# Optimization experiments

Measured on AMD Instinct MI355X. Metric: run time of the kernel, lower is better.

Reference implementation:

```python
import jax, jax.numpy as jnp
import numpy as np

STAGE = 100  # number of weight bins


def _bin_reconstruct(w, affine):
    # Faithful vectorization of the 100-iter binning loop: element in bin i
    # (half-open interval) gets scaled by affine[i]; the max element falls
    # outside every bin (w < wmin + stage*range/stage fails) and is zeroed.
    flat = w.reshape(-1)
    wmin, wmax = flat.min(), flat.max()
    idx = jnp.floor((flat - wmin) / (wmax - wmin) * STAGE).astype(jnp.int32)
    mask = (idx < STAGE).astype(flat.dtype)  # mask is detached in torch (non-diff anyway)
    scale = affine[jnp.clip(idx, 0, STAGE - 1)]
    return flat * scale * mask


def _kl_vs_laplace(new_flat, lap):
    # F.kl_div(log_softmax(w), softmax(lap), reduction='none').mean()
    logq = jax.nn.log_softmax(new_flat)
    p = jax.nn.softmax(lap)
    return (p * (jnp.log(p) - logq)).mean()


def _adder2d(x, w, stride, padding, groups=1):
    # AdderNet conv: out = -sum_k |patch_k - w_k| (no bias)
    O, Cg, kh, kw = w.shape
    patches = jax.lax.conv_general_dilated_patches(
        x, (kh, kw), (stride, stride), [(padding, padding), (padding, padding)])
    B, _, Hp, Wp = patches.shape  # channel dim ordered (C, kh, kw), C-major
    if groups == 1:
        p = patches.reshape(B, 1, Cg * kh * kw, Hp, Wp)
        wf = w.reshape(1, O, Cg * kh * kw, 1, 1)
    else:  # depthwise: groups == C_in, Cg == 1, O == C_in
        p = patches.reshape(B, O, kh * kw, Hp, Wp)
        wf = w.reshape(1, O, kh * kw, 1, 1)
    return -jnp.abs(p - wf).sum(axis=2)  # [B, O, Hp, Wp]


def _bn_train(x, g, b, eps=1e-5):
    # BatchNorm2d in training mode (batch statistics, biased variance)
    m = x.mean(axis=(0, 2, 3), keepdims=True)
    v = ((x - m) ** 2).mean(axis=(0, 2, 3), keepdims=True)
    return (x - m) * jax.lax.rsqrt(v + eps) * g.reshape(1, -1, 1, 1) + b.reshape(1, -1, 1, 1)


def _forward(x, sw_ds, sw_c1, sw_c2, sw_c3, a_ds, a_c1, a_c2, a_c3, peg_w,
             g1, b1, g2, b2, g3, b3, gds, bds, lap_ds, lap_c1, lap_c2, lap_c3):
    kl = jnp.float32(0.0)
    f_ds = _bin_reconstruct(sw_ds, a_ds)
    kl = kl + _kl_vs_laplace(f_ds, lap_ds)
    f_c1 = _bin_reconstruct(sw_c1, a_c1)
    kl = kl + _kl_vs_laplace(f_c1, lap_c1)
    residual = jax.nn.relu(_bn_train(_adder2d(x, f_ds.reshape(sw_ds.shape), 1, 0), gds, bds))
    h = _adder2d(x, f_c1.reshape(sw_c1.shape), 1, 0)
    h = _adder2d(h, peg_w, 1, 1, groups=peg_w.shape[0])  # PEG depthwise 3x3
    h = jax.nn.relu(_bn_train(h, g1, b1))
    f_c2 = _bin_reconstruct(sw_c2, a_c2)
    kl = kl + _kl_vs_laplace(f_c2, lap_c2)
    h = _adder2d(h, f_c2.reshape(sw_c2.shape), 1, 1)
    h = jax.nn.relu(_bn_train(h, g2, b2))
    f_c3 = _bin_reconstruct(sw_c3, a_c3)
    kl = kl + _kl_vs_laplace(f_c3, lap_c3)
    h = _adder2d(h, f_c3.reshape(sw_c3.shape), 1, 0)
    h = _bn_train(h, g3, b3)  # bn3 gamma zero-initialized
    return jax.nn.relu(h + residual), kl


def setup_inputs() -> dict:
    key = jax.random.key(0)
    ks = jax.random.split(key, 16)
    inp = {
        'x': jax.random.normal(ks[0], (4, 128, 28, 28), jnp.float32),
        'sw_downsample': jax.random.normal(ks[1], (256, 128, 1, 1), jnp.float32) * 0.05,
        'sw_conv1': jax.random.normal(ks[2], (64, 128, 1, 1), jnp.float32) * 0.05,
        'sw_conv2': jax.random.normal(ks[3], (64, 64, 3, 3), jnp.float32) * 0.05,
        'sw_conv3': jax.random.normal(ks[4], (256, 64, 1, 1), jnp.float32) * 0.05,
        'downsample_affine': jax.random.normal(ks[5], (100,), jnp.float32),
        'conv1_affine': jax.random.normal(ks[6], (100,), jnp.float32),
        'conv2_affine': jax.random.normal(ks[7], (100,), jnp.float32),
        'conv3_affine': jax.random.normal(ks[8], (100,), jnp.float32),
        'peg_w': jax.random.normal(ks[9], (64, 1, 3, 3), jnp.float32) * 0.05,
        'bn1_g': jnp.ones((64,), jnp.float32), 'bn1_b': jnp.zeros((64,), jnp.float32),
        'bn2_g': jnp.ones((64,), jnp.float32), 'bn2_b': jnp.zeros((64,), jnp.float32),
        'bn3_g': jnp.zeros((256,), jnp.float32), 'bn3_b': jnp.zeros((256,), jnp.float32),
        'bnds_g': jnp.ones((256,), jnp.float32), 'bnds_b': jnp.zeros((256,), jnp.float32),
        # Laplace(0, 2) samples, drawn once in setup so the reference is deterministic
        'lap_ds': jax.random.laplace(ks[10], (32768,), jnp.float32) * 2.0,
        'lap_c1': jax.random.laplace(ks[11], (8192,), jnp.float32) * 2.0,
        'lap_c2': jax.random.laplace(ks[12], (36864,), jnp.float32) * 2.0,
        'lap_c3': jax.random.laplace(ks[13], (16384,), jnp.float32) * 2.0,
    }
    return inp


def reference(x, sw_downsample, sw_conv1, sw_conv2, sw_conv3,
              downsample_affine, conv1_affine, conv2_affine, conv3_affine, peg_w,
              bn1_g, bn1_b, bn2_g, bn2_b, bn3_g, bn3_b, bnds_g, bnds_b,
              lap_ds, lap_c1, lap_c2, lap_c3):
    return _forward(x, sw_downsample, sw_conv1, sw_conv2, sw_conv3,
                    downsample_affine, conv1_affine, conv2_affine, conv3_affine, peg_w,
                    bn1_g, bn1_b, bn2_g, bn2_b, bn3_g, bn3_b, bnds_g, bnds_b,
                    lap_ds, lap_c1, lap_c2, lap_c3)
```

## Files before the change

kernel.cpp:

```cpp
#include <hip/hip_runtime.h>
#include <math.h>


#define HW 784
#define NB 4
#define STAGE 100

__device__ __forceinline__ float wredSum(float v){
  for (int o = 32; o > 0; o >>= 1) v += __shfl_down(v, o, 64);
  return v;
}
__device__ __forceinline__ float wredMax(float v){
  for (int o = 32; o > 0; o >>= 1) v = fmaxf(v, __shfl_down(v, o, 64));
  return v;
}
__device__ __forceinline__ float wredMin(float v){
  for (int o = 32; o > 0; o >>= 1) v = fminf(v, __shfl_down(v, o, 64));
  return v;
}
__device__ __forceinline__ double wredSumD(double v){
  for (int o = 32; o > 0; o >>= 1) v += __shfl_down(v, o, 64);
  return v;
}

__device__ float blockSum16(float v){
  __shared__ float sh[16];
  __syncthreads();
  v = wredSum(v);
  if ((threadIdx.x & 63) == 0) sh[threadIdx.x >> 6] = v;
  __syncthreads();
  float r = 0.0f;
  #pragma unroll
  for (int i = 0; i < 16; i++) r += sh[i];
  return r;
}
__device__ float blockMax16(float v){
  __shared__ float sh[16];
  __syncthreads();
  v = wredMax(v);
  if ((threadIdx.x & 63) == 0) sh[threadIdx.x >> 6] = v;
  __syncthreads();
  float r = sh[0];
  #pragma unroll
  for (int i = 1; i < 16; i++) r = fmaxf(r, sh[i]);
  return r;
}
__device__ float blockMin16(float v){
  __shared__ float sh[16];
  __syncthreads();
  v = wredMin(v);
  if ((threadIdx.x & 63) == 0) sh[threadIdx.x >> 6] = v;
  __syncthreads();
  float r = sh[0];
  #pragma unroll
  for (int i = 1; i < 16; i++) r = fminf(r, sh[i]);
  return r;
}

__device__ void stats4(float v0, float v1, float v2, float v3,
                       double* sumP, double* sqP, int oc0){
  __shared__ double sred[4][8];
  __syncthreads();
  const int w = threadIdx.x >> 6;
  float vv[4] = {v0, v1, v2, v3};
  #pragma unroll
  for (int i = 0; i < 4; i++){
    double d = (double)vv[i];
    double s = wredSumD(d);
    double q = wredSumD(d * d);
    if ((threadIdx.x & 63) == 0){ sred[w][i] = s; sred[w][4 + i] = q; }
  }
  __syncthreads();
  if (threadIdx.x < 8){
    double tot = sred[0][threadIdx.x] + sred[1][threadIdx.x]
               + sred[2][threadIdx.x] + sred[3][threadIdx.x];
    int i = threadIdx.x & 3;
    if (threadIdx.x < 4) atomicAdd(&sumP[oc0 + i], tot);
    else                 atomicAdd(&sqP[oc0 + i],  tot);
  }
}
__device__ void stats2(float v0, float v1, double* sumP, double* sqP, int oc0){
  __shared__ double sred2[4][4];
  __syncthreads();
  const int w = threadIdx.x >> 6;
  float vv[2] = {v0, v1};
  #pragma unroll
  for (int i = 0; i < 2; i++){
    double d = (double)vv[i];
    double s = wredSumD(d);
    double q = wredSumD(d * d);
    if ((threadIdx.x & 63) == 0){ sred2[w][i] = s; sred2[w][2 + i] = q; }
  }
  __syncthreads();
  if (threadIdx.x < 4){
    double tot = sred2[0][threadIdx.x] + sred2[1][threadIdx.x]
               + sred2[2][threadIdx.x] + sred2[3][threadIdx.x];
    int i = threadIdx.x & 1;
    if (threadIdx.x < 2) atomicAdd(&sumP[oc0 + i], tot);
    else                 atomicAdd(&sqP[oc0 + i],  tot);
  }
}

__global__ __launch_bounds__(1024) void recon_kl_kernel(
    const float* w0, const float* a0, const float* l0, float* f0, int n0,
    const float* w1, const float* a1, const float* l1, float* f1, int n1,
    const float* w2, const float* a2, const float* l2, float* f2, int n2,
    const float* w3, const float* a3, const float* l3, float* f3, int n3,
    float* kl_out, double* dstat)
{
  for (int i = threadIdx.x; i < 320; i += 1024) dstat[blockIdx.x * 320 + i] = 0.0;

  const float* w; const float* aff; const float* lap; float* f; int n;
  int t = blockIdx.x;
  if      (t == 0){ w = w0; aff = a0; lap = l0; f = f0; n = n0; }
  else if (t == 1){ w = w1; aff = a1; lap = l1; f = f1; n = n1; }
  else if (t == 2){ w = w2; aff = a2; lap = l2; f = f2; n = n2; }
  else            { w = w3; aff = a3; lap = l3; f = f3; n = n3; }

  __shared__ float saff[STAGE];
  for (int i = threadIdx.x; i < STAGE; i += 1024) saff[i] = aff[i];

  const float4* w4 = (const float4*)w;
  const float4* l4 = (const float4*)lap;
  float4*       f4 = (float4*)f;
  const int n4 = n >> 2;

  float mn = 3.402823466e38f, mx = -3.402823466e38f, ml = -3.402823466e38f;
  for (int i = threadIdx.x; i < n4; i += 1024){
    float4 v = w4[i];
    mn = fminf(mn, fminf(fminf(v.x, v.y), fminf(v.z, v.w)));
    mx = fmaxf(mx, fmaxf(fmaxf(v.x, v.y), fmaxf(v.z, v.w)));
    float4 u = l4[i];
    ml = fmaxf(ml, fmaxf(fmaxf(u.x, u.y), fmaxf(u.z, u.w)));
  }
  mn = blockMin16(mn); mx = blockMax16(mx); ml = blockMax16(ml);
  const float rng = mx - mn;

  float maxf = -3.402823466e38f;
  for (int i = threadIdx.x; i < n4; i += 1024){
    float4 v = w4[i];
    float4 o;
    float* vp = &v.x; float* op = &o.x;
    #pragma unroll
    for (int k = 0; k < 4; k++){
      float vv = vp[k];
      float q = (vv - mn) / rng * 100.0f;
      int idx = (int)floorf(q);
      float nv = 0.0f;
      if (idx < STAGE){
        int ci = idx < 0 ? 0 : (idx > STAGE - 1 ? STAGE - 1 : idx);
        nv = vv * saff[ci];
      }
      op[k] = nv;
      maxf = fmaxf(maxf, nv);
    }
    f4[i] = o;
  }
  maxf = blockMax16(maxf);

  float se = 0.0f, sel = 0.0f, sef = 0.0f, sq = 0.0f;
  for (int i = threadIdx.x; i < n4; i += 1024){
    float4 u = l4[i];
    float4 fv = f4[i];
    float* up = &u.x; float* fp = &fv.x;
    #pragma unroll
    for (int k = 0; k < 4; k++){
      float e = expf(up[k] - ml);
      se  += e;
      sel += e * up[k];
      sef += e * fp[k];
      sq  += expf(fp[k] - maxf);
    }
  }
  se  = blockSum16(se);
  sel = blockSum16(sel);
  sef = blockSum16(sef);
  sq  = blockSum16(sq);

  if (threadIdx.x == 0){
    kl_out[t] = ((sel - sef) / se - ml - logf(se) + maxf + logf(sq)) / (float)n;
  }
}

__global__ __launch_bounds__(256) void front_kernel(
    const float* __restrict__ x, const float* __restrict__ f_ds,
    const float* __restrict__ f_c1, const float* __restrict__ peg_w,
    float* __restrict__ A, float* __restrict__ T2, double* __restrict__ dS)
{
  const int t = threadIdx.x;
  if (blockIdx.x < 512){
    const int a = blockIdx.x;
    const int chunk = a & 3, og = (a >> 2) & 31, b = a >> 7;
    const int oc0 = og * 8;
    __shared__ float sw[1024];
    for (int k = t; k < 1024; k += 256) sw[k] = f_ds[oc0 * 128 + k];
    __syncthreads();
    const int px = chunk * 256 + t;
    float v0=0,v1=0,v2=0,v3=0,v4=0,v5=0,v6=0,v7=0;
    if (px < HW){
      const float* xp = x + (size_t)b * 128 * HW + px;
      float c0=0,c1=0,c2=0,c3=0,c4=0,c5=0,c6=0,c7=0;
      #pragma unroll 4
      for (int c = 0; c < 128; c++){
        float xv = xp[(size_t)c * HW];
        c0 += fabsf(xv - sw[c]);
        c1 += fabsf(xv - sw[128 + c]);
        c2 += fabsf(xv - sw[256 + c]);
        c3 += fabsf(xv - sw[384 + c]);
        c4 += fabsf(xv - sw[512 + c]);
        c5 += fabsf(xv - sw[640 + c]);
        c6 += fabsf(xv - sw[768 + c]);
        c7 += fabsf(xv - sw[896 + c]);
      }
      v0=-c0; v1=-c1; v2=-c2; v3=-c3; v4=-c4; v5=-c5; v6=-c6; v7=-c7;
      float* op = A + ((size_t)(b * 256 + oc0)) * HW + px;
      op[0]=v0; op[HW]=v1; op[2*HW]=v2; op[3*HW]=v3;
      op[4*HW]=v4; op[5*HW]=v5; op[6*HW]=v6; op[7*HW]=v7;
    }
    stats4(v0, v1, v2, v3, dS + 0, dS + 256, oc0);
    stats4(v4, v5, v6, v7, dS + 0, dS + 256, oc0 + 4);
  } else {
    const int a = blockIdx.x - 512;
    const int rc = a & 3, og = (a >> 2) & 15, b = a >> 6;
    const int oc0 = og * 4;
    __shared__ float swc[512];
    __shared__ float swp[36];
    __shared__ float sT1[4][256];
    for (int k = t; k < 512; k += 256) swc[k] = f_c1[oc0 * 128 + k];
    if (t < 36) swp[t] = peg_w[oc0 * 9 + t];
    __syncthreads();
    if (t < 252){
      const int rr = t / 28;
      const int col = t - rr * 28;
      const int wr = rc * 7 - 1 + rr;
      float tv0 = 0, tv1 = 0, tv2 = 0, tv3 = 0;
      if (wr >= 0 && wr < 28){
        const float* xp = x + (size_t)b * 128 * HW + wr * 28 + col;
        float c0 = 0, c1 = 0, c2 = 0, c3 = 0;
        #pragma unroll 4
        for (int c = 0; c < 128; c++){
          float xv = xp[(size_t)c * HW];
          c0 += fabsf(xv - swc[c]);
          c1 += fabsf(xv - swc[128 + c]);
          c2 += fabsf(xv - swc[256 + c]);
          c3 += fabsf(xv - swc[384 + c]);
        }
        tv0 = -c0; tv1 = -c1; tv2 = -c2; tv3 = -c3;
      }
      sT1[0][t] = tv0; sT1[1][t] = tv1; sT1[2][t] = tv2; sT1[3][t] = tv3;
    }
    __syncthreads();
    float v0 = 0, v1 = 0, v2 = 0, v3 = 0;
    if (t < 196){
      const int r = t / 28, col = t - r * 28;
      float c0 = 0, c1 = 0, c2 = 0, c3 = 0;
      #pragma unroll
      for (int ky = 0; ky < 3; ky++){
        #pragma unroll
        for (int kx = 0; kx < 3; kx++){
          int cc = col + kx - 1;
          bool ok = (cc >= 0) && (cc < 28);
          int idx = ok ? ((r + ky) * 28 + cc) : 0;
          float p0 = ok ? sT1[0][idx] : 0.0f;
          float p1 = ok ? sT1[1][idx] : 0.0f;
          float p2 = ok ? sT1[2][idx] : 0.0f;
          float p3 = ok ? sT1[3][idx] : 0.0f;
          int wk = ky * 3 + kx;
          c0 += fabsf(p0 - swp[wk]);
          c1 += fabsf(p1 - swp[9 + wk]);
          c2 += fabsf(p2 - swp[18 + wk]);
          c3 += fabsf(p3 - swp[27 + wk]);
        }
      }
      v0 = -c0; v1 = -c1; v2 = -c2; v3 = -c3;
      const int opx = (rc * 7 + r) * 28 + col;
      float* op = T2 + ((size_t)(b * 64 + oc0)) * HW + opx;
      op[0] = v0; op[HW] = v1; op[2 * HW] = v2; op[3 * HW] = v3;
    }
    stats4(v0, v1, v2, v3, dS + 512, dS + 576, oc0);
  }
}

__global__ __launch_bounds__(256) void bnapply_pad_kernel(
    const float* __restrict__ T2, float* __restrict__ T2b,
    const float* __restrict__ g1, const float* __restrict__ b1,
    const double* __restrict__ dS)
{
  const int a = blockIdx.x;
  const int c = a & 63, b = a >> 6;
  __shared__ float ssc, ssb;
  if (threadIdx.x == 0){
    double s  = dS[512 + c] * (1.0 / 3136.0);
    double vr = dS[576 + c] * (1.0 / 3136.0) - s * s;
    float scale = g1[c] * rsqrtf((float)vr + 1e-5f);
    ssc = scale; ssb = b1[c] - (float)s * scale;
  }
  __syncthreads();
  const float sc_ = ssc, bi_ = ssb;
  const float* src = T2 + (size_t)a * HW;
  float* dst = T2b + (size_t)a * 960;
  for (int i = threadIdx.x; i < 960; i += 256){
    int row = i >> 5, col = i & 31;
    float v = 0.0f;
    if (row >= 1 && row <= 28 && col >= 1 && col <= 28)
      v = fmaxf(src[(row - 1) * 28 + (col - 1)] * sc_ + bi_, 0.0f);
    dst[i] = v;
  }
}

__global__ __launch_bounds__(256) void mid3x3_kernel(
    const float* __restrict__ T2b, const float* __restrict__ f_c2,
    float* __restrict__ T3, double* __restrict__ dS)
{
  const int t = threadIdx.x;
  const int a = blockIdx.x;
  const int chunk = a & 3, og = (a >> 2) & 31, b = a >> 7;
  const int oc0 = og * 2;
  const float* __restrict__ wA = f_c2 + oc0 * 576;
  const float* __restrict__ wB = wA + 576;

  float v0 = 0, v1 = 0;
  const int px = chunk * 196 + t;
  if (t < 196){
    const int y = px / 28, xc = px - y * 28;
    const float* base = T2b + (size_t)b * 64 * 960 + y * 32 + xc;
    float c0 = 0, c1 = 0;
    #pragma unroll 2
    for (int c = 0; c < 64; c++){
      const float* p = base + c * 960;
      float t0 = p[0],  t1 = p[1],  t2 = p[2];
      float t3 = p[32], t4 = p[33], t5 = p[34];
      float t6 = p[64], t7 = p[65], t8 = p[66];
      const float* wa = wA + c * 9;
      const float* wb = wB + c * 9;
      c0 += fabsf(t0 - wa[0]) + fabsf(t1 - wa[1]) + fabsf(t2 - wa[2])
          + fabsf(t3 - wa[3]) + fabsf(t4 - wa[4]) + fabsf(t5 - wa[5])
          + fabsf(t6 - wa[6]) + fabsf(t7 - wa[7]) + fabsf(t8 - wa[8]);
      c1 += fabsf(t0 - wb[0]) + fabsf(t1 - wb[1]) + fabsf(t2 - wb[2])
          + fabsf(t3 - wb[3]) + fabsf(t4 - wb[4]) + fabsf(t5 - wb[5])
          + fabsf(t6 - wb[6]) + fabsf(t7 - wb[7]) + fabsf(t8 - wb[8]);
    }
    v0 = -c0; v1 = -c1;
    T3[((size_t)(b * 64 + oc0)) * HW + px]     = v0;
    T3[((size_t)(b * 64 + oc0 + 1)) * HW + px] = v1;
  }
  stats2(v0, v1, dS + 640, dS + 704, oc0);
}

__global__ __launch_bounds__(256) void back_kernel(
    const float* __restrict__ T3, const float* __restrict__ f_c3,
    const float* __restrict__ g2, const float* __restrict__ b2,
    float* __restrict__ out, double* __restrict__ dS)
{
  const int t = threadIdx.x;
  const int a = blockIdx.x;
  const int chunk = a & 3, og = (a >> 2) & 63, b = a >> 8;
  const int oc0 = og * 4;
  __shared__ float ssc[64], ssb[64], sw[256];
  if (t < 64){
    double s  = dS[640 + t] * (1.0 / 3136.0);
    double vr = dS[704 + t] * (1.0 / 3136.0) - s * s;
    float scale = g2[t] * rsqrtf((float)vr + 1e-5f);
    ssc[t] = scale; ssb[t] = b2[t] - (float)s * scale;
  }
  sw[t] = f_c3[oc0 * 64 + t];
  __syncthreads();

  const int px = chunk * 256 + t;
  float v0 = 0, v1 = 0, v2 = 0, v3 = 0;
  if (px < HW){
    const float* bp = T3 + (size_t)b * 64 * HW + px;
    float c0 = 0, c1 = 0, c2 = 0, c3 = 0;
    #pragma unroll 4
    for (int c = 0; c < 64; c++){
      float raw = bp[(size_t)c * HW];
      float vv = fmaxf(raw * ssc[c] + ssb[c], 0.0f);
      c0 += fabsf(vv - sw[c]);
      c1 += fabsf(vv - sw[64 + c]);
      c2 += fabsf(vv - sw[128 + c]);
      c3 += fabsf(vv - sw[192 + c]);
    }
    v0 = -c0; v1 = -c1; v2 = -c2; v3 = -c3;
    float* op = out + ((size_t)(b * 256 + oc0)) * HW + px;
    op[0] = v0; op[HW] = v1; op[2 * HW] = v2; op[3 * HW] = v3;
  }
  stats4(v0, v1, v2, v3, dS + 768, dS + 1024, oc0);
}

__global__ __launch_bounds__(256) void final_kernel(
    float* __restrict__ out, const float* __restrict__ A,
    const float* __restrict__ g3, const float* __restrict__ b3,
    const float* __restrict__ gds, const float* __restrict__ bds,
    const double* __restrict__ dS, const float* __restrict__ kl)
{
  __shared__ float s3c[256], s3b[256], sdc[256], sdb[256];
  const int t = threadIdx.x;
  {
    double s  = dS[768 + t] * (1.0 / 3136.0);
    double vr = dS[1024 + t] * (1.0 / 3136.0) - s * s;
    float scale = g3[t] * rsqrtf((float)vr + 1e-5f);
    s3c[t] = scale; s3b[t] = b3[t] - (float)s * scale;
    s  = dS[t] * (1.0 / 3136.0);
    vr = dS[256 + t] * (1.0 / 3136.0) - s * s;
    scale = gds[t] * rsqrtf((float)vr + 1e-5f);
    sdc[t] = scale; sdb[t] = bds[t] - (float)s * scale;
  }
  __syncthreads();
  #pragma unroll
  for (int k = 0; k < 4; k++){
    int n = blockIdx.x * 1024 + k * 256 + t;
    int c = (n / HW) & 255;
    float h = out[n], aa = A[n];
    float r = fmaxf(aa * sdc[c] + sdb[c], 0.0f);
    out[n] = fmaxf(h * s3c[c] + s3b[c] + r, 0.0f);
  }
  if (blockIdx.x == 0 && t == 0) out[802816] = kl[0] + kl[1] + kl[2] + kl[3];
}

extern "C" void kernel_launch(void* const* d_in, const int* in_sizes, int n_in,
                              void* d_out, int out_size, void* d_ws, size_t ws_size,
                              hipStream_t stream)
{
  const float* x      = (const float*)d_in[0];
  const float* sw_ds  = (const float*)d_in[1];
  const float* sw_c1  = (const float*)d_in[2];
  const float* sw_c2  = (const float*)d_in[3];
  const float* sw_c3  = (const float*)d_in[4];
  const float* a_ds   = (const float*)d_in[5];
  const float* a_c1   = (const float*)d_in[6];
  const float* a_c2   = (const float*)d_in[7];
  const float* a_c3   = (const float*)d_in[8];
  const float* peg_w  = (const float*)d_in[9];
  const float* bn1_g  = (const float*)d_in[10];
  const float* bn1_b  = (const float*)d_in[11];
  const float* bn2_g  = (const float*)d_in[12];
  const float* bn2_b  = (const float*)d_in[13];
  const float* bn3_g  = (const float*)d_in[14];
  const float* bn3_b  = (const float*)d_in[15];
  const float* bnds_g = (const float*)d_in[16];
  const float* bnds_b = (const float*)d_in[17];
  const float* lap_ds = (const float*)d_in[18];
  const float* lap_c1 = (const float*)d_in[19];
  const float* lap_c2 = (const float*)d_in[20];
  const float* lap_c3 = (const float*)d_in[21];

  float* ws    = (float*)d_ws;
  float* f_ds  = ws;
  float* f_c1  = ws + 32768;
  float* f_c2  = ws + 40960;
  float* f_c3  = ws + 77824;
  float* kl    = ws + 94208;
  double* dstat= (double*)(ws + 98304);
  float* A     = ws + 102400;
  float* T2    = ws + 905216;
  float* T3    = ws + 1105920;
  float* T2b   = ws + 1306624;

  float* out = (float*)d_out;

  recon_kl_kernel<<<4, 1024, 0, stream>>>(
      sw_ds, a_ds, lap_ds, f_ds, 32768,
      sw_c1, a_c1, lap_c1, f_c1, 8192,
      sw_c2, a_c2, lap_c2, f_c2, 36864,
      sw_c3, a_c3, lap_c3, f_c3, 16384, kl, dstat);

  front_kernel<<<768, 256, 0, stream>>>(x, f_ds, f_c1, peg_w, A, T2, dstat);

  bnapply_pad_kernel<<<256, 256, 0, stream>>>(T2, T2b, bn1_g, bn1_b, dstat);

  mid3x3_kernel<<<512, 256, 0, stream>>>(T2b, f_c2, T3, dstat);

  back_kernel<<<1024, 256, 0, stream>>>(T3, f_c3, bn2_g, bn2_b, out, dstat);

  final_kernel<<<784, 256, 0, stream>>>(out, A, bn3_g, bn3_b, bnds_g, bnds_b,
                                        dstat, kl);
}
```

Measured before the change: 188.2 us.

## Split weight min/max into parallel kernel and fuse reconstruction and KL into consumers

The serial 4-block recon+KL kernel becomes a 64-block min/max kernel. Weight reconstruction now happens on the fly inside front_kernel and back_kernel. The KL partial sums are computed by a few designated and extra front_kernel blocks and accumulated with double atomics. The KL drops the max-subtraction for stability and relies on unshifted exp sums. Pixel chunking changes from 256 to 196 per block, so no threads sit idle past the image end.

```diff
diff --git a/kernel.cpp b/kernel.cpp
--- a/kernel.cpp
+++ b/kernel.cpp
@@ -23,38 +23,21 @@
   return v;
 }
 
-__device__ float blockSum16(float v){
-  __shared__ float sh[16];
-  __syncthreads();
-  v = wredSum(v);
-  if ((threadIdx.x & 63) == 0) sh[threadIdx.x >> 6] = v;
-  __syncthreads();
-  float r = 0.0f;
-  #pragma unroll
-  for (int i = 0; i < 16; i++) r += sh[i];
-  return r;
-}
-__device__ float blockMax16(float v){
-  __shared__ float sh[16];
+__device__ float blockMin4(float v){
+  __shared__ float shn[4];
+  __syncthreads();
+  v = wredMin(v);
+  if ((threadIdx.x & 63) == 0) shn[threadIdx.x >> 6] = v;
+  __syncthreads();
+  return fminf(fminf(shn[0], shn[1]), fminf(shn[2], shn[3]));
+}
+__device__ float blockMax4(float v){
+  __shared__ float shx[4];
   __syncthreads();
   v = wredMax(v);
-  if ((threadIdx.x & 63) == 0) sh[threadIdx.x >> 6] = v;
-  __syncthreads();
-  float r = sh[0];
-  #pragma unroll
-  for (int i = 1; i < 16; i++) r = fmaxf(r, sh[i]);
-  return r;
-}
-__device__ float blockMin16(float v){
-  __shared__ float sh[16];
-  __syncthreads();
-  v = wredMin(v);
-  if ((threadIdx.x & 63) == 0) sh[threadIdx.x >> 6] = v;
-  __syncthreads();
-  float r = sh[0];
-  #pragma unroll
-  for (int i = 1; i < 16; i++) r = fminf(r, sh[i]);
-  return r;
+  if ((threadIdx.x & 63) == 0) shx[threadIdx.x >> 6] = v;
+  __syncthreads();
+  return fmaxf(fmaxf(shx[0], shx[1]), fmaxf(shx[2], shx[3]));
 }
 
 __device__ void stats4(float v0, float v1, float v2, float v3,
@@ -101,90 +84,82 @@
   }
 }
 
-__global__ __launch_bounds__(1024) void recon_kl_kernel(
-    const float* w0, const float* a0, const float* l0, float* f0, int n0,
-    const float* w1, const float* a1, const float* l1, float* f1, int n1,
-    const float* w2, const float* a2, const float* l2, float* f2, int n2,
-    const float* w3, const float* a3, const float* l3, float* f3, int n3,
-    float* kl_out, double* dstat)
-{
-  for (int i = threadIdx.x; i < 320; i += 1024) dstat[blockIdx.x * 320 + i] = 0.0;
-
-  const float* w; const float* aff; const float* lap; float* f; int n;
-  int t = blockIdx.x;
-  if      (t == 0){ w = w0; aff = a0; lap = l0; f = f0; n = n0; }
-  else if (t == 1){ w = w1; aff = a1; lap = l1; f = f1; n = n1; }
-  else if (t == 2){ w = w2; aff = a2; lap = l2; f = f2; n = n2; }
-  else            { w = w3; aff = a3; lap = l3; f = f3; n = n3; }
-
-  __shared__ float saff[STAGE];
-  for (int i = threadIdx.x; i < STAGE; i += 1024) saff[i] = aff[i];
-
-  const float4* w4 = (const float4*)w;
-  const float4* l4 = (const float4*)lap;
-  float4*       f4 = (float4*)f;
-  const int n4 = n >> 2;
-
-  float mn = 3.402823466e38f, mx = -3.402823466e38f, ml = -3.402823466e38f;
-  for (int i = threadIdx.x; i < n4; i += 1024){
-    float4 v = w4[i];
-    mn = fminf(mn, fminf(fminf(v.x, v.y), fminf(v.z, v.w)));
-    mx = fmaxf(mx, fmaxf(fmaxf(v.x, v.y), fmaxf(v.z, v.w)));
-    float4 u = l4[i];
-    ml = fmaxf(ml, fmaxf(fmaxf(u.x, u.y), fmaxf(u.z, u.w)));
-  }
-  mn = blockMin16(mn); mx = blockMax16(mx); ml = blockMax16(ml);
-  const float rng = mx - mn;
-
-  float maxf = -3.402823466e38f;
-  for (int i = threadIdx.x; i < n4; i += 1024){
-    float4 v = w4[i];
-    float4 o;
-    float* vp = &v.x; float* op = &o.x;
-    #pragma unroll
-    for (int k = 0; k < 4; k++){
-      float vv = vp[k];
-      float q = (vv - mn) / rng * 100.0f;
-      int idx = (int)floorf(q);
-      float nv = 0.0f;
-      if (idx < STAGE){
-        int ci = idx < 0 ? 0 : (idx > STAGE - 1 ? STAGE - 1 : idx);
-        nv = vv * saff[ci];
-      }
-      op[k] = nv;
-      maxf = fmaxf(maxf, nv);
-    }
-    f4[i] = o;
-  }
-  maxf = blockMax16(maxf);
-
-  float se = 0.0f, sel = 0.0f, sef = 0.0f, sq = 0.0f;
-  for (int i = threadIdx.x; i < n4; i += 1024){
-    float4 u = l4[i];
-    float4 fv = f4[i];
-    float* up = &u.x; float* fp = &fv.x;
-    #pragma unroll
-    for (int k = 0; k < 4; k++){
-      float e = expf(up[k] - ml);
-      se  += e;
-      sel += e * up[k];
-      sef += e * fp[k];
-      sq  += expf(fp[k] - maxf);
-    }
-  }
-  se  = blockSum16(se);
-  sel = blockSum16(sel);
-  sef = blockSum16(sef);
-  sq  = blockSum16(sq);
-
+__device__ void klAccum(float se, float sel, float sef, float sq, double* dst){
+  __shared__ double kls[4][4];
+  __syncthreads();
+  const int w = threadIdx.x >> 6;
+  double a0 = wredSumD((double)se);
+  double a1 = wredSumD((double)sel);
+  double a2 = wredSumD((double)sef);
+  double a3 = wredSumD((double)sq);
+  if ((threadIdx.x & 63) == 0){
+    kls[w][0] = a0; kls[w][1] = a1; kls[w][2] = a2; kls[w][3] = a3;
+  }
+  __syncthreads();
+  if (threadIdx.x < 4){
+    double tot = kls[0][threadIdx.x] + kls[1][threadIdx.x]
+               + kls[2][threadIdx.x] + kls[3][threadIdx.x];
+    atomicAdd(&dst[threadIdx.x], tot);
+  }
+}
+
+__device__ __forceinline__ float reconv(float vv, float mn, float rng,
+                                        const float* saff){
+  float q = (vv - mn) / rng * 100.0f;
+  int idx = (int)floorf(q);
+  float nv = 0.0f;
+  if (idx < STAGE){
+    int ci = idx < 0 ? 0 : (idx > STAGE - 1 ? STAGE - 1 : idx);
+    nv = vv * saff[ci];
+  }
+  return nv;
+}
+
+__device__ __forceinline__ void mmReduce(const float* mmbuf, int tens,
+                                         float& mn, float& mx){
+  mn = 3.402823466e38f; mx = -3.402823466e38f;
+  #pragma unroll
+  for (int k = 0; k < 16; k++){
+    mn = fminf(mn, mmbuf[tens * 32 + k]);
+    mx = fmaxf(mx, mmbuf[tens * 32 + 16 + k]);
+  }
+}
+
+__global__ __launch_bounds__(256) void minmax_kernel(
+    const float* w0, int n0, const float* w1, int n1,
+    const float* w2, int n2, const float* w3, int n3,
+    float* mmbuf, double* dstat)
+{
+  if (threadIdx.x < 21) dstat[blockIdx.x * 21 + threadIdx.x] = 0.0;
+  const int tens = blockIdx.x >> 4, slot = blockIdx.x & 15;
+  const float* w; int n;
+  if      (tens == 0){ w = w0; n = n0; }
+  else if (tens == 1){ w = w1; n = n1; }
+  else if (tens == 2){ w = w2; n = n2; }
+  else               { w = w3; n = n3; }
+  float mn = 3.402823466e38f, mx = -3.402823466e38f;
+  for (int i = slot * 256 + threadIdx.x; i < n; i += 4096){
+    float v = w[i];
+    mn = fminf(mn, v); mx = fmaxf(mx, v);
+  }
+  mn = blockMin4(mn); mx = blockMax4(mx);
   if (threadIdx.x == 0){
-    kl_out[t] = ((sel - sef) / se - ml - logf(se) + maxf + logf(sq)) / (float)n;
+    mmbuf[tens * 32 + slot]      = mn;
+    mmbuf[tens * 32 + 16 + slot] = mx;
   }
 }
 
 __global__ __launch_bounds__(256) void front_kernel(
-    const float* __restrict__ x, const float* __restrict__ f_ds,
-    const float* __restrict__ f_c1, const float* __restrict__ peg_w,
+    const float* __restrict__ x,
+    const float* __restrict__ w_ds, const float* __restrict__ aff_ds,
+    const float* __restrict__ lap_ds,
+    const float* __restrict__ w_c1, const float* __restrict__ aff_c1,
+    const float* __restrict__ lap_c1,
+    const float* __restrict__ w_c2, const float* __restrict__ aff_c2,
+    const float* __restrict__ lap_c2, float* __restrict__ f_c2,
+    const float* __restrict__ w_c3, const float* __restrict__ aff_c3,
+    const float* __restrict__ lap_c3,
+    const float* __restrict__ peg_w, const float* __restrict__ mmbuf,
     float* __restrict__ A, float* __restrict__ T2, double* __restrict__ dS)
 {
   const int t = threadIdx.x;
@@ -192,12 +167,19 @@
     const int a = blockIdx.x;
     const int chunk = a & 3, og = (a >> 2) & 31, b = a >> 7;
     const int oc0 = og * 8;
+    __shared__ float saff[STAGE];
     __shared__ float sw[1024];
-    for (int k = t; k < 1024; k += 256) sw[k] = f_ds[oc0 * 128 + k];
-    __syncthreads();
-    const int px = chunk * 256 + t;
+    if (t < STAGE) saff[t] = aff_ds[t];
+    float mn, mx; mmReduce(mmbuf, 0, mn, mx);
+    const float rng = mx - mn;
+    __syncthreads();
+    for (int k = t; k < 1024; k += 256)
+      sw[k] = reconv(w_ds[oc0 * 128 + k], mn, rng, saff);
+    __syncthreads();
+
+    const int px = chunk * 196 + t;
     float v0=0,v1=0,v2=0,v3=0,v4=0,v5=0,v6=0,v7=0;
-    if (px < HW){
+    if (t < 196){
       const float* xp = x + (size_t)b * 128 * HW + px;
       float c0=0,c1=0,c2=0,c3=0,c4=0,c5=0,c6=0,c7=0;
       #pragma unroll 4
@@ -219,16 +201,34 @@
     }
     stats4(v0, v1, v2, v3, dS + 0, dS + 256, oc0);
     stats4(v4, v5, v6, v7, dS + 0, dS + 256, oc0 + 4);
-  } else {
+
+    if (b == 0 && chunk == 0){
+      float se = 0, sel = 0, sef = 0, sq = 0;
+      for (int k = t; k < 1024; k += 256){
+        float l = lap_ds[oc0 * 128 + k];
+        float e = expf(l);
+        se += e; sel += e * l; sef += e * sw[k];
+        sq += expf(sw[k]);
+      }
+      klAccum(se, sel, sef, sq, dS + 1280 + 0);
+    }
+  } else if (blockIdx.x < 768){
     const int a = blockIdx.x - 512;
     const int rc = a & 3, og = (a >> 2) & 15, b = a >> 6;
     const int oc0 = og * 4;
+    __shared__ float saffc[STAGE];
     __shared__ float swc[512];
     __shared__ float swp[36];
     __shared__ float sT1[4][256];
-    for (int k = t; k < 512; k += 256) swc[k] = f_c1[oc0 * 128 + k];
-    if (t < 36) swp[t] = peg_w[oc0 * 9 + t];
-    __syncthreads();
+    if (t < STAGE) saffc[t] = aff_c1[t];
+    if (t >= 128 && t < 164) swp[t - 128] = peg_w[oc0 * 9 + (t - 128)];
+    float mn, mx; mmReduce(mmbuf, 1, mn, mx);
+    const float rng = mx - mn;
+    __syncthreads();
+    for (int k = t; k < 512; k += 256)
+      swc[k] = reconv(w_c1[oc0 * 128 + k], mn, rng, saffc);
+    __syncthreads();
+
     if (t < 252){
       const int rr = t / 28;
       const int col = t - rr * 28;
@@ -278,6 +278,48 @@
       op[0] = v0; op[HW] = v1; op[2 * HW] = v2; op[3 * HW] = v3;
     }
     stats4(v0, v1, v2, v3, dS + 512, dS + 576, oc0);
+
+    if (b == 0 && rc == 0){
+      float se = 0, sel = 0, sef = 0, sq = 0;
+      for (int k = t; k < 512; k += 256){
+        float l = lap_c1[oc0 * 128 + k];
+        float e = expf(l);
+        se += e; sel += e * l; sef += e * swc[k];
+        sq += expf(swc[k]);
+      }
+      klAccum(se, sel, sef, sq, dS + 1280 + 4);
+    }
+  } else if (blockIdx.x < 832){
+    const int j = blockIdx.x - 768;
+    __shared__ float saff2[STAGE];
+    if (t < STAGE) saff2[t] = aff_c2[t];
+    float mn, mx; mmReduce(mmbuf, 2, mn, mx);
+    const float rng = mx - mn;
+    __syncthreads();
+    float se = 0, sel = 0, sef = 0, sq = 0;
+    for (int k = t; k < 576; k += 256){
+      float nv = reconv(w_c2[j * 576 + k], mn, rng, saff2);
+      f_c2[j * 576 + k] = nv;
+      float l = lap_c2[j * 576 + k];
+      float e = expf(l);
+      se += e; sel += e * l; sef += e * nv; sq += expf(nv);
+    }
+    klAccum(se, sel, sef, sq, dS + 1280 + 8);
+  } else {
+    const int j = blockIdx.x - 832;
+    __shared__ float saff3[STAGE];
+    if (t < STAGE) saff3[t] = aff_c3[t];
+    float mn, mx; mmReduce(mmbuf, 3, mn, mx);
+    const float rng = mx - mn;
+    __syncthreads();
+    float se = 0, sel = 0, sef = 0, sq = 0;
+    for (int k = t; k < 1024; k += 256){
+      float nv = reconv(w_c3[j * 1024 + k], mn, rng, saff3);
+      float l = lap_c3[j * 1024 + k];
+      float e = expf(l);
+      se += e; sel += e * l; sef += e * nv; sq += expf(nv);
+    }
+    klAccum(se, sel, sef, sq, dS + 1280 + 12);
   }
 }
 
@@ -348,7 +390,8 @@
 }
 
 __global__ __launch_bounds__(256) void back_kernel(
-    const float* __restrict__ T3, const float* __restrict__ f_c3,
+    const float* __restrict__ T3, const float* __restrict__ w_c3,
+    const float* __restrict__ aff_c3, const float* __restrict__ mmbuf,
     const float* __restrict__ g2, const float* __restrict__ b2,
     float* __restrict__ out, double* __restrict__ dS)
 {
@@ -356,19 +399,23 @@
   const int a = blockIdx.x;
   const int chunk = a & 3, og = (a >> 2) & 63, b = a >> 8;
   const int oc0 = og * 4;
-  __shared__ float ssc[64], ssb[64], sw[256];
+  __shared__ float ssc[64], ssb[64], sw[256], saff[STAGE];
   if (t < 64){
     double s  = dS[640 + t] * (1.0 / 3136.0);
     double vr = dS[704 + t] * (1.0 / 3136.0) - s * s;
     float scale = g2[t] * rsqrtf((float)vr + 1e-5f);
     ssc[t] = scale; ssb[t] = b2[t] - (float)s * scale;
   }
-  sw[t] = f_c3[oc0 * 64 + t];
-  __syncthreads();
-
-  const int px = chunk * 256 + t;
+  if (t >= 128 && t < 128 + STAGE) saff[t - 128] = aff_c3[t - 128];
+  float mn, mx; mmReduce(mmbuf, 3, mn, mx);
+  const float rng = mx - mn;
+  __syncthreads();
+  sw[t] = reconv(w_c3[oc0 * 64 + t], mn, rng, saff);
+  __syncthreads();
+
+  const int px = chunk * 196 + t;
   float v0 = 0, v1 = 0, v2 = 0, v3 = 0;
-  if (px < HW){
+  if (t < 196){
     const float* bp = T3 + (size_t)b * 64 * HW + px;
     float c0 = 0, c1 = 0, c2 = 0, c3 = 0;
     #pragma unroll 4
@@ -391,7 +438,7 @@
     float* __restrict__ out, const float* __restrict__ A,
     const float* __restrict__ g3, const float* __restrict__ b3,
     const float* __restrict__ gds, const float* __restrict__ bds,
-    const double* __restrict__ dS, const float* __restrict__ kl)
+    const double* __restrict__ dS)
 {
   __shared__ float s3c[256], s3b[256], sdc[256], sdb[256];
   const int t = threadIdx.x;
@@ -414,7 +461,19 @@
     float r = fmaxf(aa * sdc[c] + sdb[c], 0.0f);
     out[n] = fmaxf(h * s3c[c] + s3b[c] + r, 0.0f);
   }
-  if (blockIdx.x == 0 && t == 0) out[802816] = kl[0] + kl[1] + kl[2] + kl[3];
+  if (blockIdx.x == 0 && t == 0){
+    const int ns[4] = {32768, 8192, 36864, 16384};
+    float kl = 0.0f;
+    #pragma unroll
+    for (int q = 0; q < 4; q++){
+      double se  = dS[1280 + q * 4];
+      double sel = dS[1280 + q * 4 + 1];
+      double sef = dS[1280 + q * 4 + 2];
+      double sq  = dS[1280 + q * 4 + 3];
+      kl += (float)((((sel - sef) / se) - log(se) + log(sq)) / (double)ns[q]);
+    }
+    out[802816] = kl;
+  }
 }
 
 extern "C" void kernel_launch(void* const* d_in, const int* in_sizes, int n_in,
@@ -445,33 +504,31 @@
   const float* lap_c3 = (const float*)d_in[21];
 
   float* ws    = (float*)d_ws;
-  float* f_ds  = ws;
-  float* f_c1  = ws + 32768;
-  float* f_c2  = ws + 40960;
-  float* f_c3  = ws + 77824;
-  float* kl    = ws + 94208;
-  double* dstat= (double*)(ws + 98304);
-  float* A     = ws + 102400;
-  float* T2    = ws + 905216;
-  float* T3    = ws + 1105920;
-  float* T2b   = ws + 1306624;
+  float* f_c2  = ws;
+  float* mmbuf = ws + 36864;
+  double* dstat= (double*)(ws + 37120);
+  float* A     = ws + 39808;
+  float* T2    = ws + 842624;
+  float* T3    = ws + 1043328;
+  float* T2b   = ws + 1244032;
 
   float* out = (float*)d_out;
 
-  recon_kl_kernel<<<4, 1024, 0, stream>>>(
-      sw_ds, a_ds, lap_ds, f_ds, 32768,
-      sw_c1, a_c1, lap_c1, f_c1, 8192,
-      sw_c2, a_c2, lap_c2, f_c2, 36864,
-      sw_c3, a_c3, lap_c3, f_c3, 16384, kl, dstat);
-
-  front_kernel<<<768, 256, 0, stream>>>(x, f_ds, f_c1, peg_w, A, T2, dstat);
+  minmax_kernel<<<64, 256, 0, stream>>>(
+      sw_ds, 32768, sw_c1, 8192, sw_c2, 36864, sw_c3, 16384, mmbuf, dstat);
+
+  front_kernel<<<848, 256, 0, stream>>>(
+      x, sw_ds, a_ds, lap_ds, sw_c1, a_c1, lap_c1,
+      sw_c2, a_c2, lap_c2, f_c2, sw_c3, a_c3, lap_c3,
+      peg_w, mmbuf, A, T2, dstat);
 
   bnapply_pad_kernel<<<256, 256, 0, stream>>>(T2, T2b, bn1_g, bn1_b, dstat);
 
   mid3x3_kernel<<<512, 256, 0, stream>>>(T2b, f_c2, T3, dstat);
 
-  back_kernel<<<1024, 256, 0, stream>>>(T3, f_c3, bn2_g, bn2_b, out, dstat);
+  back_kernel<<<1024, 256, 0, stream>>>(T3, sw_c3, a_c3, mmbuf,
+                                        bn2_g, bn2_b, out, dstat);
 
   final_kernel<<<784, 256, 0, stream>>>(out, A, bn3_g, bn3_b, bnds_g, bnds_b,
-                                        dstat, kl);
-}
+                                        dstat);
+}
```

After: 171.8 us. -8.7%, faster.
